# Performance work log

Hardware: AMD Instinct MI355X
Metric: run time of the kernel (lower is better)

## Reference

```python
import jax, jax.numpy as jnp
import numpy as np

D_MODEL = 1024
NUM_HEADS = 16
HEAD_DIM = D_MODEL // NUM_HEADS


def setup_inputs() -> dict:
    key = jax.random.key(0)
    k_x, k_wqkv, k_bqkv, k_wo, k_bo = jax.random.split(key, 5)
    bound_qkv = 1.0 / np.sqrt(D_MODEL)
    x = jax.random.normal(k_x, (2, 2048, D_MODEL), dtype=jnp.float32)
    # torch nn.Linear init: U(-1/sqrt(fan_in), 1/sqrt(fan_in))
    W_qkv = jax.random.uniform(k_wqkv, (D_MODEL, 3 * D_MODEL), jnp.float32, -bound_qkv, bound_qkv)
    b_qkv = jax.random.uniform(k_bqkv, (3 * D_MODEL,), jnp.float32, -bound_qkv, bound_qkv)
    W_out = jax.random.uniform(k_wo, (D_MODEL, D_MODEL), jnp.float32, -bound_qkv, bound_qkv)
    b_out = jax.random.uniform(k_bo, (D_MODEL,), jnp.float32, -bound_qkv, bound_qkv)
    return {"x": x, "W_qkv": W_qkv, "b_qkv": b_qkv, "W_out": W_out, "b_out": b_out}


def reference(x, W_qkv, b_qkv, W_out, b_out):
    B, T, C = x.shape
    H, Dh = NUM_HEADS, HEAD_DIM
    qkv = x @ W_qkv + b_qkv                      # [B,T,3C]
    q, k, v = jnp.split(qkv, 3, axis=-1)
    # [B,T,C] -> [B,H,T,Dh]
    def to_heads(t):
        return t.reshape(B, T, H, Dh).transpose(0, 2, 1, 3)
    q, k, v = to_heads(q), to_heads(k), to_heads(v)
    scale = 1.0 / np.sqrt(Dh).astype(np.float32)
    scores = jnp.einsum("bhqd,bhkd->bhqk", q, k) * scale   # [B,H,T,T]
    weights = jax.nn.softmax(scores, axis=-1)
    attn = jnp.einsum("bhqk,bhkd->bhqd", weights, v)        # [B,H,T,Dh]
    attn = attn.transpose(0, 2, 1, 3).reshape(B, T, C)
    return attn @ W_out + b_out
```

## Files before the change

kernel.cpp:

```cpp
#include <hip/hip_runtime.h>

typedef __bf16 bf16x8 __attribute__((ext_vector_type(8)));
typedef float f32x4 __attribute__((ext_vector_type(4)));
typedef float f32x16 __attribute__((ext_vector_type(16)));

#define MFMA16(a, b, c) __builtin_amdgcn_mfma_f32_16x16x32_bf16(a, b, c, 0, 0, 0)
#define MFMA32(a, b, c) __builtin_amdgcn_mfma_f32_32x32x16_bf16(a, b, c, 0, 0, 0)
#define GLDS16(g, l)                                                              \
  __builtin_amdgcn_global_load_lds((const __attribute__((address_space(1))) void*)(g), \
                                   (__attribute__((address_space(3))) void*)(l), 16, 0, 0)

__global__ __launch_bounds__(256) void cvt_bf16_kernel(const float* __restrict__ in,
                                                       __bf16* __restrict__ out, int n4) {
  int i = blockIdx.x * 256 + threadIdx.x;
  if (i < n4) {
    float4 v = ((const float4*)in)[i];
    union { __bf16 b[4]; uint2 u; } t;
    t.b[0] = (__bf16)v.x; t.b[1] = (__bf16)v.y;
    t.b[2] = (__bf16)v.z; t.b[3] = (__bf16)v.w;
    ((uint2*)out)[i] = t.u;
  }
}

__global__ __launch_bounds__(256) void transpose_w_kernel(const float* __restrict__ Wq,
                                                          __bf16* __restrict__ WqT,
                                                          const float* __restrict__ Wo,
                                                          __bf16* __restrict__ WoT) {
  const int Kd = 1024;
  int bx = blockIdx.x;
  const float* W; __bf16* WT; int Nd, n0;
  if (bx < 96) { W = Wq; WT = WqT; Nd = 3072; n0 = bx * 32; }
  else         { W = Wo; WT = WoT; Nd = 1024; n0 = (bx - 96) * 32; }
  __shared__ float tile[32][33];
  int k0 = blockIdx.y * 32;
  int tid = threadIdx.x;
  int kk = tid >> 3, nn = (tid & 7) * 4;
  float4 v = *(const float4*)&W[(size_t)(k0 + kk) * Nd + n0 + nn];
  tile[kk][nn] = v.x; tile[kk][nn + 1] = v.y;
  tile[kk][nn + 2] = v.z; tile[kk][nn + 3] = v.w;
  __syncthreads();
  int n2 = tid >> 3, k2 = (tid & 7) * 4;
  union { __bf16 b[4]; uint2 u; } t;
  t.b[0] = (__bf16)tile[k2][n2];
  t.b[1] = (__bf16)tile[k2 + 1][n2];
  t.b[2] = (__bf16)tile[k2 + 2][n2];
  t.b[3] = (__bf16)tile[k2 + 3][n2];
  *(uint2*)&WT[(size_t)(n0 + n2) * Kd + k0 + k2] = t.u;
}

template <bool OUT_F32, int NT>
__global__ __launch_bounds__(256) void gemm_kernel(const __bf16* __restrict__ A,
                                                   const __bf16* __restrict__ BT,
                                                   const float* __restrict__ bias,
                                                   void* __restrict__ Cout, int N,
                                                   int qn, float qs) {
  const int K = 1024;
  const int NJ = NT / 32;
  __shared__ __align__(16) __bf16 As[128 * 32];
  __shared__ __align__(16) __bf16 Bs[NT * 32];
  int tid = threadIdx.x;
  int wave = tid >> 6, lane = tid & 63;
  int quad = lane >> 4, l16 = lane & 15;
  int m0 = blockIdx.x * 128, n0 = blockIdx.y * NT;
  int wm = (wave >> 1) * 64, wn = (wave & 1) * (NT / 2);

  int srow = tid >> 2, scol = (tid & 3) * 8;
  const __bf16* aptr = A + (size_t)(m0 + srow) * K + scol;
  const __bf16* bptr = BT + (size_t)(n0 + srow) * K + scol;
  __bf16* asl = &As[(size_t)wave * 512];
  __bf16* bsl = &Bs[(size_t)wave * 512];

  f32x4 acc[4][NJ] = {};
  for (int k0 = 0; k0 < K; k0 += 32) {
    GLDS16(aptr + k0, asl);
    GLDS16(aptr + (size_t)64 * K + k0, asl + 2048);
    GLDS16(bptr + k0, bsl);
    if (NT == 128) GLDS16(bptr + (size_t)64 * K + k0, bsl + 2048);
    __syncthreads();
    bf16x8 af[4], bf[NJ];
    for (int i = 0; i < 4; i++)
      af[i] = *(bf16x8*)&As[(wm + i * 16 + l16) * 32 + quad * 8];
    for (int j = 0; j < NJ; j++)
      bf[j] = *(bf16x8*)&Bs[(wn + j * 16 + l16) * 32 + quad * 8];
    for (int i = 0; i < 4; i++)
      for (int j = 0; j < NJ; j++)
        acc[i][j] = MFMA16(af[i], bf[j], acc[i][j]);
    __syncthreads();
  }
  for (int j = 0; j < NJ; j++) {
    int col = n0 + wn + j * 16 + l16;
    float bv = bias[col];
    float sc = (col < qn) ? qs : 1.0f;
    for (int i = 0; i < 4; i++) {
      int rowb = m0 + wm + i * 16 + quad * 4;
      for (int r = 0; r < 4; r++) {
        float v = (acc[i][j][r] + bv) * sc;
        if (OUT_F32)
          ((float*)Cout)[(size_t)(rowb + r) * N + col] = v;
        else
          ((__bf16*)Cout)[(size_t)(rowb + r) * N + col] = (__bf16)v;
      }
    }
  }
}

__global__ __launch_bounds__(256) void transpose_v_kernel(const __bf16* __restrict__ qkv,
                                                          __bf16* __restrict__ Vt) {
  const int T = 2048, C3 = 3072;
  __shared__ __align__(16) __bf16 tile[64][72];
  int t0 = blockIdx.x * 64;
  int h = blockIdx.y, b = blockIdx.z;
  int tid = threadIdx.x;
  int tt = tid >> 2, c = (tid & 3) * 16;
  const __bf16* src = qkv + (size_t)(b * T + t0 + tt) * C3 + 2048 + h * 64 + c;
  *(uint4*)&tile[tt][c] = *(const uint4*)src;
  *(uint4*)&tile[tt][c + 8] = *(const uint4*)(src + 8);
  __syncthreads();
  int dd = tid >> 2, t2 = (tid & 3) * 16;
  union { __bf16 b_[16]; uint4 u[2]; } o;
  for (int i = 0; i < 16; i++) o.b_[i] = tile[t2 + i][dd];
  __bf16* dst = Vt + ((size_t)(b * 16 + h) * 64 + dd) * T + t0 + t2;
  *(uint4*)dst = o.u[0];
  *(uint4*)(dst + 8) = o.u[1];
}

__global__ __launch_bounds__(128) void attn_kernel(const __bf16* __restrict__ qkv,
                                                   const __bf16* __restrict__ Vt,
                                                   __bf16* __restrict__ O) {
  const int T = 2048, C3 = 3072;
  int q0 = blockIdx.x * 64;
  int h = blockIdx.y, b = blockIdx.z;
  int tid = threadIdx.x, wave = tid >> 6, lane = tid & 63;
  int l31 = lane & 31, hw = lane >> 5;

  __shared__ __align__(16) __bf16 KV[2][8192];
  __shared__ __align__(16) __bf16 Ps[2][2048];

  const __bf16* qp = qkv + (size_t)(b * T + q0 + wave * 32 + l31) * C3 + h * 64 + hw * 8;
  bf16x8 aq[4];
  for (int c = 0; c < 4; c++) aq[c] = *(const bf16x8*)(qp + c * 16);

  const __bf16* kbase = qkv + (size_t)(b * T) * C3 + 1024 + h * 64;
  const __bf16* vbase = Vt + (size_t)(b * 16 + h) * 64 * T;

  const __bf16* ksrc = kbase + (size_t)l31 * C3 + hw * 8;
  const __bf16* vsrc = vbase + (size_t)l31 * T + hw * 8;

  int kchi = (lane >> 4) & 1, rh = (lane >> 3) & 1, jj = lane & 7;
  int wbase = kchi * 512 + rh * 256 + (hw ^ rh) * 32 + jj;
  int rbase = hw * 256 + (l31 ^ (hw * 4)) * 8;

  f32x16 o0 = {}, o1 = {}, ls = {};
  bf16x8 ones;
  for (int i = 0; i < 8; i++) ones[i] = (__bf16)1.0f;

  if (wave == 0) {
    for (int ct = 0; ct < 2; ct++)
      for (int c = 0; c < 4; c++)
        GLDS16(ksrc + (size_t)ct * 32 * C3 + c * 16, &KV[0][(ct * 4 + c) * 512]);
  } else {
    for (int kc = 0; kc < 4; kc++)
      for (int dt = 0; dt < 2; dt++)
        GLDS16(vsrc + (size_t)dt * 32 * T + kc * 16, &KV[0][4096 + (kc * 2 + dt) * 512]);
  }

  for (int t0 = 0; t0 < T; t0 += 64) {
    int buf = (t0 >> 6) & 1;
    __syncthreads();

    if (t0 + 64 < T) {
      if (wave == 0) {
        const __bf16* ks = ksrc + (size_t)(t0 + 64) * C3;
        for (int ct = 0; ct < 2; ct++)
          for (int c = 0; c < 4; c++)
            GLDS16(ks + (size_t)ct * 32 * C3 + c * 16, &KV[buf ^ 1][(ct * 4 + c) * 512]);
      } else {
        const __bf16* vs = vsrc + t0 + 64;
        for (int kc = 0; kc < 4; kc++)
          for (int dt = 0; dt < 2; dt++)
            GLDS16(vs + (size_t)dt * 32 * T + kc * 16,
                   &KV[buf ^ 1][4096 + (kc * 2 + dt) * 512]);
      }
    }

    const __bf16* Kb = &KV[buf][0];
    const __bf16* Vb = &KV[buf][4096];

    for (int ct = 0; ct < 2; ct++) {
      f32x16 ss = {};
      for (int c = 0; c < 4; c++) {
        bf16x8 bk = *(const bf16x8*)&Kb[(ct * 4 + c) * 512 + lane * 8];
        ss = MFMA32(aq[c], bk, ss);
      }
#pragma unroll
      for (int reg = 0; reg < 16; reg++) {
        int dq = (reg & 3) + 8 * (reg >> 2);
        float p = __builtin_amdgcn_exp2f(ss[reg]);
        Ps[wave][wbase + ct * 1024 + dq * 8] = (__bf16)p;
      }
    }

    for (int kc = 0; kc < 4; kc++) {
      bf16x8 ap = *(const bf16x8*)&Ps[wave][rbase + kc * 512];
      ls = MFMA32(ap, ones, ls);
      bf16x8 bv0 = *(const bf16x8*)&Vb[(kc * 2 + 0) * 512 + lane * 8];
      bf16x8 bv1 = *(const bf16x8*)&Vb[(kc * 2 + 1) * 512 + lane * 8];
      o0 = MFMA32(ap, bv0, o0);
      o1 = MFMA32(ap, bv1, o1);
    }
  }

  __bf16* obase = O + (size_t)(b * T + q0 + wave * 32 + 4 * hw) * 1024 + h * 64 + l31;
#pragma unroll
  for (int reg = 0; reg < 16; reg++) {
    int dq = (reg & 3) + 8 * (reg >> 2);
    float inv = 1.0f / ls[reg];
    obase[(size_t)dq * 1024] = (__bf16)(o0[reg] * inv);
    obase[(size_t)dq * 1024 + 32] = (__bf16)(o1[reg] * inv);
  }
}

extern "C" void kernel_launch(void* const* d_in, const int* in_sizes, int n_in,
                              void* d_out, int out_size, void* d_ws, size_t ws_size,
                              hipStream_t stream) {
  const float* x = (const float*)d_in[0];
  const float* W_qkv = (const float*)d_in[1];
  const float* b_qkv = (const float*)d_in[2];
  const float* W_out = (const float*)d_in[3];
  const float* b_out = (const float*)d_in[4];
  float* out = (float*)d_out;

  char* ws = (char*)d_ws;
  __bf16* WqkvT = (__bf16*)(ws);
  __bf16* WoT = (__bf16*)(ws + 6291456);
  __bf16* xb = (__bf16*)(ws + 8388608);
  __bf16* qkvb = (__bf16*)(ws + 16777216);
  __bf16* Vt = (__bf16*)(ws + 41943040);
  __bf16* attnb = xb;

  const float cs = 0.125f * 1.44269504089f;

  cvt_bf16_kernel<<<4096, 256, 0, stream>>>(x, xb, 1048576);
  transpose_w_kernel<<<dim3(128, 32), 256, 0, stream>>>(W_qkv, WqkvT, W_out, WoT);
  gemm_kernel<false, 128><<<dim3(32, 24), 256, 0, stream>>>(xb, WqkvT, b_qkv, qkvb, 3072,
                                                            1024, cs);
  transpose_v_kernel<<<dim3(32, 16, 2), 256, 0, stream>>>(qkvb, Vt);
  attn_kernel<<<dim3(32, 16, 2), 128, 0, stream>>>(qkvb, Vt, attnb);
  gemm_kernel<true, 64><<<dim3(32, 16), 256, 0, stream>>>(attnb, WoT, b_out, out, 1024,
                                                          0, 1.0f);
}
```

Before: 209.8 us.

## Keep attention probabilities in registers via transposed S and bpermute; double K-step in GEMM

The attention kernel now computes S transposed (K as the A operand), so the exp'd probabilities land in registers in a layout usable as the A operand of the PV MFMA after a cross-half-wave ds_bpermute swap. This removes the shared-memory round trip for P and the extra MFMA against a ones vector for row sums, which are now accumulated in scalar registers and exchanged once at the end. Separately, the GEMM loads two 32-wide K slices per barrier pair, halving the number of synchronisations per K sweep at the cost of doubled LDS use. The cost is added bpermute/select instructions and a shuffle per output register in the epilogue.

```diff
diff --git a/kernel.cpp b/kernel.cpp
--- a/kernel.cpp
+++ b/kernel.cpp
@@ -9,6 +9,12 @@
 #define GLDS16(g, l)                                                              \
   __builtin_amdgcn_global_load_lds((const __attribute__((address_space(1))) void*)(g), \
                                    (__attribute__((address_space(3))) void*)(l), 16, 0, 0)
+
+static __device__ __forceinline__ unsigned pack_bf16(float a, float b) {
+  union { __bf16 h[2]; unsigned u; } t;
+  t.h[0] = (__bf16)a; t.h[1] = (__bf16)b;
+  return t.u;
+}
 
 __global__ __launch_bounds__(256) void cvt_bf16_kernel(const float* __restrict__ in,
                                                        __bf16* __restrict__ out, int n4) {
@@ -56,8 +62,8 @@
                                                    int qn, float qs) {
   const int K = 1024;
   const int NJ = NT / 32;
-  __shared__ __align__(16) __bf16 As[128 * 32];
-  __shared__ __align__(16) __bf16 Bs[NT * 32];
+  __shared__ __align__(16) __bf16 As[2][128 * 32];
+  __shared__ __align__(16) __bf16 Bs[2][NT * 32];
   int tid = threadIdx.x;
   int wave = tid >> 6, lane = tid & 63;
   int quad = lane >> 4, l16 = lane & 15;
@@ -67,24 +73,28 @@
   int srow = tid >> 2, scol = (tid & 3) * 8;
   const __bf16* aptr = A + (size_t)(m0 + srow) * K + scol;
   const __bf16* bptr = BT + (size_t)(n0 + srow) * K + scol;
-  __bf16* asl = &As[(size_t)wave * 512];
-  __bf16* bsl = &Bs[(size_t)wave * 512];
 
   f32x4 acc[4][NJ] = {};
-  for (int k0 = 0; k0 < K; k0 += 32) {
-    GLDS16(aptr + k0, asl);
-    GLDS16(aptr + (size_t)64 * K + k0, asl + 2048);
-    GLDS16(bptr + k0, bsl);
-    if (NT == 128) GLDS16(bptr + (size_t)64 * K + k0, bsl + 2048);
+  for (int k0 = 0; k0 < K; k0 += 64) {
+#pragma unroll
+    for (int kh = 0; kh < 2; kh++) {
+      GLDS16(aptr + k0 + kh * 32, &As[kh][wave * 512]);
+      GLDS16(aptr + (size_t)64 * K + k0 + kh * 32, &As[kh][wave * 512 + 2048]);
+      GLDS16(bptr + k0 + kh * 32, &Bs[kh][wave * 512]);
+      if (NT == 128) GLDS16(bptr + (size_t)64 * K + k0 + kh * 32, &Bs[kh][wave * 512 + 2048]);
+    }
     __syncthreads();
-    bf16x8 af[4], bf[NJ];
-    for (int i = 0; i < 4; i++)
-      af[i] = *(bf16x8*)&As[(wm + i * 16 + l16) * 32 + quad * 8];
-    for (int j = 0; j < NJ; j++)
-      bf[j] = *(bf16x8*)&Bs[(wn + j * 16 + l16) * 32 + quad * 8];
-    for (int i = 0; i < 4; i++)
+#pragma unroll
+    for (int kh = 0; kh < 2; kh++) {
+      bf16x8 af[4], bf[NJ];
+      for (int i = 0; i < 4; i++)
+        af[i] = *(bf16x8*)&As[kh][(wm + i * 16 + l16) * 32 + quad * 8];
       for (int j = 0; j < NJ; j++)
-        acc[i][j] = MFMA16(af[i], bf[j], acc[i][j]);
+        bf[j] = *(bf16x8*)&Bs[kh][(wn + j * 16 + l16) * 32 + quad * 8];
+      for (int i = 0; i < 4; i++)
+        for (int j = 0; j < NJ; j++)
+          acc[i][j] = MFMA16(af[i], bf[j], acc[i][j]);
+    }
     __syncthreads();
   }
   for (int j = 0; j < NJ; j++) {
@@ -132,33 +142,30 @@
   int h = blockIdx.y, b = blockIdx.z;
   int tid = threadIdx.x, wave = tid >> 6, lane = tid & 63;
   int l31 = lane & 31, hw = lane >> 5;
+  int perm = (lane ^ 32) << 2;
 
   __shared__ __align__(16) __bf16 KV[2][8192];
-  __shared__ __align__(16) __bf16 Ps[2][2048];
 
   const __bf16* qp = qkv + (size_t)(b * T + q0 + wave * 32 + l31) * C3 + h * 64 + hw * 8;
-  bf16x8 aq[4];
-  for (int c = 0; c < 4; c++) aq[c] = *(const bf16x8*)(qp + c * 16);
+  bf16x8 bq[4];
+#pragma unroll
+  for (int c = 0; c < 4; c++) bq[c] = *(const bf16x8*)(qp + c * 16);
 
   const __bf16* kbase = qkv + (size_t)(b * T) * C3 + 1024 + h * 64;
   const __bf16* vbase = Vt + (size_t)(b * 16 + h) * 64 * T;
-
   const __bf16* ksrc = kbase + (size_t)l31 * C3 + hw * 8;
   const __bf16* vsrc = vbase + (size_t)l31 * T + hw * 8;
 
-  int kchi = (lane >> 4) & 1, rh = (lane >> 3) & 1, jj = lane & 7;
-  int wbase = kchi * 512 + rh * 256 + (hw ^ rh) * 32 + jj;
-  int rbase = hw * 256 + (l31 ^ (hw * 4)) * 8;
-
-  f32x16 o0 = {}, o1 = {}, ls = {};
-  bf16x8 ones;
-  for (int i = 0; i < 8; i++) ones[i] = (__bf16)1.0f;
+  f32x16 o0 = {}, o1 = {};
+  float ls_acc = 0.f;
 
   if (wave == 0) {
-    for (int ct = 0; ct < 2; ct++)
+#pragma unroll
+    for (int tt = 0; tt < 2; tt++)
       for (int c = 0; c < 4; c++)
-        GLDS16(ksrc + (size_t)ct * 32 * C3 + c * 16, &KV[0][(ct * 4 + c) * 512]);
+        GLDS16(ksrc + (size_t)tt * 32 * C3 + c * 16, &KV[0][(tt * 4 + c) * 512]);
   } else {
+#pragma unroll
     for (int kc = 0; kc < 4; kc++)
       for (int dt = 0; dt < 2; dt++)
         GLDS16(vsrc + (size_t)dt * 32 * T + kc * 16, &KV[0][4096 + (kc * 2 + dt) * 512]);
@@ -171,11 +178,13 @@
     if (t0 + 64 < T) {
       if (wave == 0) {
         const __bf16* ks = ksrc + (size_t)(t0 + 64) * C3;
-        for (int ct = 0; ct < 2; ct++)
+#pragma unroll
+        for (int tt = 0; tt < 2; tt++)
           for (int c = 0; c < 4; c++)
-            GLDS16(ks + (size_t)ct * 32 * C3 + c * 16, &KV[buf ^ 1][(ct * 4 + c) * 512]);
+            GLDS16(ks + (size_t)tt * 32 * C3 + c * 16, &KV[buf ^ 1][(tt * 4 + c) * 512]);
       } else {
         const __bf16* vs = vsrc + t0 + 64;
+#pragma unroll
         for (int kc = 0; kc < 4; kc++)
           for (int dt = 0; dt < 2; dt++)
             GLDS16(vs + (size_t)dt * 32 * T + kc * 16,
@@ -186,37 +195,61 @@
     const __bf16* Kb = &KV[buf][0];
     const __bf16* Vb = &KV[buf][4096];
 
-    for (int ct = 0; ct < 2; ct++) {
-      f32x16 ss = {};
-      for (int c = 0; c < 4; c++) {
-        bf16x8 bk = *(const bf16x8*)&Kb[(ct * 4 + c) * 512 + lane * 8];
-        ss = MFMA32(aq[c], bk, ss);
+    f32x16 sst0 = {}, sst1 = {};
+#pragma unroll
+    for (int c = 0; c < 4; c++) {
+      bf16x8 kf0 = *(const bf16x8*)&Kb[(0 * 4 + c) * 512 + lane * 8];
+      bf16x8 kf1 = *(const bf16x8*)&Kb[(1 * 4 + c) * 512 + lane * 8];
+      sst0 = MFMA32(kf0, bq[c], sst0);
+      sst1 = MFMA32(kf1, bq[c], sst1);
+    }
+
+    unsigned P2[2][4][2];
+#pragma unroll
+    for (int o = 0; o < 4; o++)
+#pragma unroll
+      for (int h2 = 0; h2 < 2; h2++) {
+        float a0 = __builtin_amdgcn_exp2f(sst0[o * 4 + h2 * 2]);
+        float a1 = __builtin_amdgcn_exp2f(sst0[o * 4 + h2 * 2 + 1]);
+        float b0 = __builtin_amdgcn_exp2f(sst1[o * 4 + h2 * 2]);
+        float b1 = __builtin_amdgcn_exp2f(sst1[o * 4 + h2 * 2 + 1]);
+        ls_acc += (a0 + a1) + (b0 + b1);
+        P2[0][o][h2] = pack_bf16(a0, a1);
+        P2[1][o][h2] = pack_bf16(b0, b1);
       }
-#pragma unroll
-      for (int reg = 0; reg < 16; reg++) {
-        int dq = (reg & 3) + 8 * (reg >> 2);
-        float p = __builtin_amdgcn_exp2f(ss[reg]);
-        Ps[wave][wbase + ct * 1024 + dq * 8] = (__bf16)p;
-      }
-    }
-
+
+#pragma unroll
     for (int kc = 0; kc < 4; kc++) {
-      bf16x8 ap = *(const bf16x8*)&Ps[wave][rbase + kc * 512];
-      ls = MFMA32(ap, ones, ls);
+      const int tt = kc >> 1, i2 = kc & 1;
+      unsigned w00 = P2[tt][2 * i2][0], w01 = P2[tt][2 * i2][1];
+      unsigned w10 = P2[tt][2 * i2 + 1][0], w11 = P2[tt][2 * i2 + 1][1];
+      unsigned s00 = (unsigned)__builtin_amdgcn_ds_bpermute(perm, (int)w00);
+      unsigned s01 = (unsigned)__builtin_amdgcn_ds_bpermute(perm, (int)w01);
+      unsigned s10 = (unsigned)__builtin_amdgcn_ds_bpermute(perm, (int)w10);
+      unsigned s11 = (unsigned)__builtin_amdgcn_ds_bpermute(perm, (int)w11);
+      union { unsigned u[4]; bf16x8 v; } pw;
+      pw.u[0] = hw ? s10 : w00;
+      pw.u[1] = hw ? s11 : w01;
+      pw.u[2] = hw ? w10 : s00;
+      pw.u[3] = hw ? w11 : s01;
       bf16x8 bv0 = *(const bf16x8*)&Vb[(kc * 2 + 0) * 512 + lane * 8];
       bf16x8 bv1 = *(const bf16x8*)&Vb[(kc * 2 + 1) * 512 + lane * 8];
-      o0 = MFMA32(ap, bv0, o0);
-      o1 = MFMA32(ap, bv1, o1);
-    }
-  }
-
-  __bf16* obase = O + (size_t)(b * T + q0 + wave * 32 + 4 * hw) * 1024 + h * 64 + l31;
+      o0 = MFMA32(pw.v, bv0, o0);
+      o1 = MFMA32(pw.v, bv1, o1);
+    }
+  }
+
+  int lsp = __builtin_amdgcn_ds_bpermute(perm, __builtin_bit_cast(int, ls_acc));
+  float ls_tot = ls_acc + __builtin_bit_cast(float, lsp);
+
+  __bf16* obase = O + (size_t)(b * T + q0 + wave * 32) * 1024 + h * 64 + l31;
 #pragma unroll
   for (int reg = 0; reg < 16; reg++) {
-    int dq = (reg & 3) + 8 * (reg >> 2);
-    float inv = 1.0f / ls[reg];
-    obase[(size_t)dq * 1024] = (__bf16)(o0[reg] * inv);
-    obase[(size_t)dq * 1024 + 32] = (__bf16)(o1[reg] * inv);
+    int q = (reg & 3) + 8 * (reg >> 2) + 4 * hw;
+    float lq = __shfl(ls_tot, q, 64);
+    float inv = 1.0f / lq;
+    obase[(size_t)q * 1024] = (__bf16)(o0[reg] * inv);
+    obase[(size_t)q * 1024 + 32] = (__bf16)(o1[reg] * inv);
   }
 }
 
```

Result: slower. 225.1 us (+7.3%).
